# Performance work log

Measured on AMD Instinct MI355X. Metric: run time of the kernel, lower is better.

The kernel has to match this reference:

```python
import jax, jax.numpy as jnp
import numpy as np

G_RATIO = 0.5
TMAX = 0.25
TB_FACTOR = 0.001


def conv2d(x, w, b):
    # x: [B,C,H,W], w: [O,C,kh,kw]
    y = jax.lax.conv_general_dilated(x, w, (1, 1), 'SAME',
                                     dimension_numbers=('NCHW', 'OIHW', 'NCHW'))
    return y + b[None, :, None, None]


def encoder(inputs, w1, b1, w2, b2):
    # simplified cost-map encoder standing in for smp.Unet; outputs sigmoid cost map [B,1,H,W]
    h = jax.nn.relu(conv2d(inputs, w1, b1))
    return jax.nn.sigmoid(conv2d(h, w2, b2))


def get_heuristic(goal_maps, tb_factor=TB_FACTOR):
    # goal_maps: [B,H,W] one-hot
    B, H, W = goal_maps.shape
    yy, xx = jnp.meshgrid(jnp.arange(H), jnp.arange(W), indexing='ij')
    loc = jnp.stack([yy, xx], 0).astype(goal_maps.dtype)          # [2,H,W]
    goal_loc = jnp.einsum('kij,bij->bk', loc, goal_maps)           # [B,2]
    d = jnp.abs(loc[None] - goal_loc[:, :, None, None])            # [B,2,H,W]
    h = d.min(axis=1) + d.max(axis=1)                              # chebyshev-style
    euc = jnp.sqrt((d ** 2).sum(axis=1))
    return h + tb_factor * euc


def st_softmax_noexp(val):
    # straight-through hard selection of the max-probability node
    B = val.shape[0]
    v = val.reshape(B, -1)
    y = v / v.sum(-1, keepdims=True)
    ind = jnp.argmax(y, axis=-1)
    y_hard = jax.nn.one_hot(ind, y.shape[-1], dtype=y.dtype)
    return (jax.lax.stop_gradient(y_hard - y) + y).reshape(val.shape)


def backtrack(start_maps, goal_maps, parents, current_t):
    B, H, W = start_maps.shape
    par = jax.lax.stop_gradient(parents).astype(jnp.int32)         # [B,HW]
    goal_flat = goal_maps.reshape(B, -1).astype(jnp.int32)
    path = goal_flat
    loc = (par * goal_flat).sum(-1)                                # parent of goal node
    rng = jnp.arange(B)

    def body(i, carry):
        path, loc = carry
        path = path.at[rng, loc].set(1)
        loc = par[rng, loc]
        return (path, loc)

    path, _ = jax.lax.fori_loop(0, current_t, body, (path, loc))
    return path.reshape(B, H, W).astype(jnp.float32)


def differentiable_astar(cost_maps, start_maps, goal_maps, obstacles_maps):
    cost = cost_maps[:, 0]
    start = start_maps[:, 0]
    goal = goal_maps[:, 0]
    obs = obstacles_maps[:, 0]
    B, H, W = cost.shape

    # Moore (8-neighbor) expansion filter: 3x3 ones with zero center
    nf = jnp.ones((1, 1, 3, 3), cost.dtype).at[0, 0, 1, 1].set(0.0)

    def expand(x):  # x: [B,H,W]
        return jax.lax.conv_general_dilated(x[:, None], nf, (1, 1), 'SAME',
                                            dimension_numbers=('NCHW', 'OIHW', 'NCHW'))[:, 0]

    h = get_heuristic(goal) + cost
    size = W
    steps = int(TMAX * H * W)
    inv_sqrt = 1.0 / np.sqrt(size)

    goal_idx = jnp.argmax(goal.reshape(B, -1), -1).astype(cost.dtype)
    parents0 = jnp.broadcast_to(goal_idx[:, None], (B, H * W)).astype(cost.dtype)
    one = jnp.asarray(1.0, cost.dtype)

    def step(carry, _):
        g, open_m, hist, parents = carry
        f = G_RATIO * g + (1.0 - G_RATIO) * h
        f_exp = jnp.exp(-f * inv_sqrt) * open_m
        sel = st_softmax_noexp(f_exp)                              # [B,H,W]

        dist_to_goal = (sel * goal).sum((1, 2), keepdims=True)
        is_unsolved = (dist_to_goal < 1e-8).astype(cost.dtype)

        hist = jnp.clip(hist + sel, 0.0, 1.0)
        open_m = jnp.clip(open_m - is_unsolved * sel, 0.0, 1.0)

        nbr = expand(sel) * obs
        g2 = expand((g + cost) * sel)
        idx = ((one - open_m) * (one - hist) + open_m * (g > g2).astype(cost.dtype)) * nbr
        idx = jax.lax.stop_gradient(idx)
        g = g2 * idx + g * (one - idx)
        g = jax.lax.stop_gradient(g)                               # detach_g=True
        open_m = jax.lax.stop_gradient(jnp.clip(open_m + idx, 0.0, 1.0))

        idx_f = idx.reshape(B, -1)
        new_par = jnp.argmax(sel.reshape(B, -1), -1).astype(cost.dtype)[:, None]
        parents = new_par * idx_f + parents * (one - idx_f)
        return (g, open_m, hist, parents), None

    init = (jnp.zeros_like(cost), start, jnp.zeros_like(cost), parents0)
    (g, open_m, hist, parents), _ = jax.lax.scan(step, init, None, length=steps)

    paths = backtrack(start, goal, parents, steps - 1)
    return hist[:, None], paths[:, None]


def setup_inputs() -> dict:
    key = jax.random.key(0)
    k1, k2, k3, k4, k5 = jax.random.split(key, 5)
    B, H, W = 64, 32, 32
    maps = (jax.random.uniform(k1, (B, 1, H, W)) > 0.15).astype(jnp.float32)  # 1 = free
    sidx = jax.random.randint(k2, (B,), 0, H * W)
    gidx = jax.random.randint(k3, (B,), 0, H * W)
    start = jax.nn.one_hot(sidx, H * W, dtype=jnp.float32).reshape(B, 1, H, W)
    goal = jax.nn.one_hot(gidx, H * W, dtype=jnp.float32).reshape(B, 1, H, W)
    maps = jnp.clip(maps + start + goal, 0.0, 1.0)  # ensure start/goal are free
    w1 = jax.random.normal(k4, (32, 2, 3, 3), jnp.float32) * 0.1
    b1 = jnp.zeros((32,), jnp.float32)
    w2 = jax.random.normal(k5, (1, 32, 3, 3), jnp.float32) * 0.1
    b2 = jnp.zeros((1,), jnp.float32)
    return {"map_designs": maps, "start_maps": start, "goal_maps": goal,
            "w1": w1, "b1": b1, "w2": w2, "b2": b2}


def reference(map_designs, start_maps, goal_maps, w1, b1, w2, b2):
    # encoder_input='m+': concat map with start+goal
    inputs = jnp.concatenate([map_designs, start_maps + goal_maps], axis=1)
    pred_cost_maps = encoder(inputs, w1, b1, w2, b2)
    obstacles_maps = map_designs  # ignore_obstacles=True, learn_obstacles=False
    histories, paths = differentiable_astar(pred_cost_maps, start_maps, goal_maps, obstacles_maps)
    return histories, paths, pred_cost_maps
```

## Files before the change

kernel.cpp:

```cpp
#include <hip/hip_runtime.h>


#define HW 1024

#define DPPMAX32(v, ctrl) do {                                                 \
    unsigned int _s = (unsigned int)__builtin_amdgcn_update_dpp(               \
        (int)(v), (int)(v), (ctrl), 0xf, 0xf, false);                          \
    (v) = (_s > (v)) ? _s : (v);                                               \
} while (0)

#define PAIR_FIX(a_) { bool _r = vr[2*(a_)+1] > vr[2*(a_)];                    \
    pv[(a_)] = _r ? vr[2*(a_)+1] : vr[2*(a_)];                                 \
    pj[(a_)] = _r ? (unsigned)(2*(a_)+1) : (unsigned)(2*(a_)); }
#define QUAD_FIX(q_) { bool _r = pv[2*(q_)+1] > pv[2*(q_)];                    \
    qv[(q_)] = _r ? pv[2*(q_)+1] : pv[2*(q_)];                                 \
    qj[(q_)] = _r ? pj[2*(q_)+1] : pj[2*(q_)]; }
#define OCT_FIX(o_) { bool _r = qv[2*(o_)+1] > qv[2*(o_)];                     \
    ov[(o_)] = _r ? qv[2*(o_)+1] : qv[2*(o_)];                                 \
    oj[(o_)] = _r ? qj[2*(o_)+1] : qj[2*(o_)]; }
#define ROOT_FIX() { bool _r = ov[1] > ov[0];                                  \
    rv = _r ? ov[1] : ov[0]; rj = _r ? oj[1] : oj[0]; }

#define ASTAR_ARM(J) {                                                         \
    constexpr int JN = ((J) < 15) ? (J) + 1 : 15;                              \
    const float gj0 = gr[(J)], hj0v = hr[(J)], cj0 = cr[(J)];                  \
    const float gj1 = gr[JN],  hj1v = hr[JN],  cj1 = cr[JN];                   \
    float gselv = jS_is_j0 ? gj0 : gj1;                                        \
    float cselv = jS_is_j0 ? cj0 : cj1;                                        \
    float gs = __uint_as_float((unsigned int)__builtin_amdgcn_readlane(        \
        (int)__float_as_uint(gselv), owner));                                  \
    float cs = __uint_as_float((unsigned int)__builtin_amdgcn_readlane(        \
        (int)__float_as_uint(cselv), owner));                                  \
    const float gsum = gs + cs;            \
    const float gA = vjA_is_j0 ? gj0 : gj1;                                    \
    const float hA = vjA_is_j0 ? hj0v : hj1v;                                  \
    const float gB = jP_is_j0 ? gj0 : gj1;                                     \
    const float hB = jP_is_j0 ? hj0v : hj1v;                                   \
    idxA = canAn || (canAr && (gA > gsum));                                    \
    idxB = canBn || (canBr && (gB > gsum));                                    \
    float fA = 0.5f * (gsum + hA);                                             \
    unsigned int nvA = __float_as_uint(expf(__fmul_rn(-fA, C_INV)));           \
    float fB = 0.5f * (gsum + hB);                                             \
    unsigned int nvB = __float_as_uint(expf(__fmul_rn(-fB, C_INV)));           \
    const bool uA0 = idxA && vjA_is_j0, uB0 = idxB && jP_is_j0;                \
    const bool uA1 = idxA && !vjA_is_j0, uB1 = idxB && !jP_is_j0;              \
    const bool u0 = uA0 || uB0, u1 = uA1 || uB1;                               \
    if (u0) { gr[(J)] = gsum; vr[(J)] = uA0 ? nvA : nvB; }                     \
    if (u1) { gr[JN]  = gsum; vr[JN]  = uA1 ? nvA : nvB; }                     \
    if (closeU &&  jS_is_j0) vr[(J)] = 0u;                                     \
    if (closeU && !jS_is_j0) vr[JN]  = 0u;                                     \
    constexpr int pa = (J) >> 1, pb = JN >> 1;                                 \
    PAIR_FIX(pa);                                                              \
    if constexpr (pb != pa) PAIR_FIX(pb);                                      \
    constexpr int qa = pa >> 1, qb = pb >> 1;                                  \
    QUAD_FIX(qa);                                                              \
    if constexpr (qb != qa) QUAD_FIX(qb);                                      \
    constexpr int oa = qa >> 1, ob = qb >> 1;                                  \
    OCT_FIX(oa);                                                               \
    if constexpr (ob != oa) OCT_FIX(ob);                                       \
    ROOT_FIX();                                                                \
  }

__global__ __launch_bounds__(256) void fused_nastar(
    const float* __restrict__ maps, const float* __restrict__ start,
    const float* __restrict__ goal, const float* __restrict__ w1,
    const float* __restrict__ b1, const float* __restrict__ w2,
    const float* __restrict__ b2, float* __restrict__ out_hist,
    float* __restrict__ out_path, float* __restrict__ out_cost) {
  __shared__ float hid[8][HW];
  __shared__ float c_l[HW];
  __shared__ unsigned short par[HW];
  __shared__ unsigned char path_sh[HW];
  __shared__ unsigned int hist_lds[64];

  const int t = threadIdx.x;
  const int b = blockIdx.x;
  const float C_INV = 0.17677669529663687f;

  const float* m_p = maps  + b * HW;
  const float* s_p = start + b * HW;
  const float* g_p = goal  + b * HW;

  float acc2[4] = {b2[0], b2[0], b2[0], b2[0]};
  for (int grp = 0; grp < 4; ++grp) {
    #pragma unroll
    for (int p = 0; p < 4; ++p) {
      int pix = p * 256 + t;
      int y = pix >> 5, x = pix & 31;
      float win0[9], win1[9];
      #pragma unroll
      for (int ky = 0; ky < 3; ++ky) {
        #pragma unroll
        for (int kx = 0; kx < 3; ++kx) {
          int yy = y + ky - 1, xx = x + kx - 1;
          bool ok = (yy >= 0) && (yy <= 31) && (xx >= 0) && (xx <= 31);
          int q = ok ? yy * 32 + xx : 0;
          float v0 = m_p[q];
          float v1 = s_p[q] + g_p[q];
          win0[ky * 3 + kx] = ok ? v0 : 0.0f;
          win1[ky * 3 + kx] = ok ? v1 : 0.0f;
        }
      }
      #pragma unroll
      for (int ocl = 0; ocl < 8; ++ocl) {
        int oc = grp * 8 + ocl;
        const float* w = w1 + oc * 18;
        float acc = b1[oc];
        #pragma unroll
        for (int k = 0; k < 9; ++k) {
          acc += win0[k] * w[k];
          acc += win1[k] * w[9 + k];
        }
        hid[ocl][pix] = fmaxf(acc, 0.0f);
      }
    }
    __syncthreads();
    #pragma unroll
    for (int p = 0; p < 4; ++p) {
      int pix = p * 256 + t;
      int y = pix >> 5, x = pix & 31;
      float a = acc2[p];
      #pragma unroll
      for (int ocl = 0; ocl < 8; ++ocl) {
        int ic = grp * 8 + ocl;
        const float* w = w2 + ic * 9;
        #pragma unroll
        for (int ky = 0; ky < 3; ++ky) {
          #pragma unroll
          for (int kx = 0; kx < 3; ++kx) {
            int yy = y + ky - 1, xx = x + kx - 1;
            bool ok = (yy >= 0) && (yy <= 31) && (xx >= 0) && (xx <= 31);
            int q = ok ? yy * 32 + xx : 0;
            float hv = hid[ocl][q];
            a += (ok ? hv : 0.0f) * w[ky * 3 + kx];
          }
        }
      }
      acc2[p] = a;
    }
    __syncthreads();
  }
  #pragma unroll
  for (int p = 0; p < 4; ++p) {
    int pix = p * 256 + t;
    float c = 1.0f / (1.0f + expf(-acc2[p]));
    c_l[pix] = c;
    out_cost[b * HW + pix] = c;
  }
  __syncthreads();

  if (t < 64) {
    const int lane = t;
    reinterpret_cast<int4*>(path_sh)[lane] = make_int4(0, 0, 0, 0);
    int myg = -1;
    #pragma unroll
    for (int j = 0; j < 16; ++j) {
      int cell = j * 64 + lane;
      if (g_p[cell] > 0.5f) myg = cell;
    }
    unsigned long long gm = __ballot(myg >= 0);
    int src_lane = (int)__ffsll(gm) - 1;
    const int goal_idx = __shfl(myg, src_lane, 64);
    const int gy = goal_idx >> 5, gx = goal_idx & 31;

    unsigned int open_m = 0, hist_m = 0, obs_m = 0;
    float gr[16], hr[16], cr[16];
    unsigned int vr[16];
    #pragma unroll
    for (int j = 0; j < 16; ++j) {
      int cell = j * 64 + lane;
      int y = cell >> 5, x = cell & 31;
      float cst = c_l[cell];
      cr[j] = cst;
      int dy = y - gy; dy = dy < 0 ? -dy : dy;
      int dx = x - gx; dx = dx < 0 ? -dx : dx;
      float e = sqrtf((float)(dy * dy + dx * dx));
      float heur = __fadd_rn((float)(dy + dx), __fmul_rn(0.001f, e));
      float hc = __fadd_rn(heur, cst);
      hr[j] = hc;
      gr[j] = 0.0f;
      bool isobs = (m_p[cell] != 0.0f);
      bool isst  = (s_p[cell] > 0.5f);
      if (isobs) obs_m  |= 1u << j;
      if (isst)  open_m |= 1u << j;
      float f = 0.5f * (0.0f + hc);
      float ex = expf(__fmul_rn(-f, C_INV));
      vr[j] = isst ? __float_as_uint(ex) : 0u;
      par[cell] = (unsigned short)goal_idx;
    }

    unsigned int pv[8], pj[8], qv[4], qj[4], ov[2], oj[2], rv, rj;
    #pragma unroll
    for (int a = 0; a < 8; ++a) PAIR_FIX(a);
    #pragma unroll
    for (int q = 0; q < 4; ++q) QUAD_FIX(q);
    #pragma unroll
    for (int o = 0; o < 2; ++o) OCT_FIX(o);
    ROOT_FIX();

    const int x = lane & 31, half = lane >> 5;
    const unsigned int lowbase = 1023u - (unsigned)lane;

    for (int step = 0; step < 256; ++step) {
      unsigned int vmx = rv;
      DPPMAX32(vmx, 0x111);
      DPPMAX32(vmx, 0x112);
      DPPMAX32(vmx, 0x114);
      DPPMAX32(vmx, 0x118);
      DPPMAX32(vmx, 0x142);
      DPPMAX32(vmx, 0x143);
      const unsigned int svmax =
          (unsigned int)__builtin_amdgcn_readlane((int)vmx, 63);

      const unsigned long long tied = __ballot(rv == svmax);
      int sel_;
      if (__popcll(tied) == 1) {
        const int wl = (int)__ffsll(tied) - 1;
        const unsigned int rjw =
            (unsigned int)__builtin_amdgcn_readlane((int)rj, wl);
        sel_ = (int)((rjw << 6) | (unsigned)wl);
      } else {
        unsigned int lo = (rv == svmax) ? (lowbase - (rj << 6)) : 0u;
        DPPMAX32(lo, 0x111);
        DPPMAX32(lo, 0x112);
        DPPMAX32(lo, 0x114);
        DPPMAX32(lo, 0x118);
        DPPMAX32(lo, 0x142);
        DPPMAX32(lo, 0x143);
        const unsigned int klo =
            (unsigned int)__builtin_amdgcn_readlane((int)lo, 63);
        sel_ = 1023 - (int)klo;
      }
      const int sel = __builtin_amdgcn_readfirstlane(sel_);
      const int jsel = sel >> 6, owner = sel & 63;
      const int ys = sel >> 5, xs = sel & 31;
      const bool unsolved = (sel != goal_idx);

      const int j0 = (ys > 0 ? ys - 1 : 0) >> 1;
      const int jP = (ys < 31 ? ys + 1 : 31) >> 1;
      const bool jS_is_j0 = (jsel == j0);
      const bool jP_is_j0 = (jP == j0);

      int dxs = x - xs; int adx = dxs < 0 ? -dxs : dxs;
      const bool act = (adx <= 1);
      const bool samep = (((ys ^ half) & 1) == 0);
      const int yA = samep ? ys : (ys - 1);
      const bool vAv = act && (samep ? (adx >= 1) : (yA >= 0));
      const int yB = ys + 1;
      const bool vBv = act && (!samep) && (yB <= 31);
      const int cA = vAv ? (yA * 32 + x) : 0;
      const int cB = vBv ? (yB * 32 + x) : 0;
      const int vjA = samep ? jsel : j0;
      const bool vjA_is_j0 = (!samep) || jS_is_j0;

      bool obA = (obs_m  >> (vjA & 15)) & 1;
      bool opA = (open_m >> (vjA & 15)) & 1;
      bool hiA = (hist_m >> (vjA & 15)) & 1;
      bool obB = (obs_m  >> (jP & 15)) & 1;
      bool opB = (open_m >> (jP & 15)) & 1;
      bool hiB = (hist_m >> (jP & 15)) & 1;
      const bool canAn = vAv && obA && !opA && !hiA;
      const bool canAr = vAv && obA && opA;
      const bool canBn = vBv && obB && !opB && !hiB;
      const bool canBr = vBv && obB && opB;

      const bool ownerlane = (lane == owner);
      const bool closeU = unsolved && ownerlane;
      const bool histnew = ownerlane && !((hist_m >> (jsel & 15)) & 1);
      const bool opencl  = closeU && ((open_m >> (jsel & 15)) & 1);

      bool idxA = false, idxB = false;

      if (j0 < 8) {
        if (j0 < 4) {
          if (j0 < 2) { if (j0 == 0) ASTAR_ARM(0) else ASTAR_ARM(1) }
          else        { if (j0 == 2) ASTAR_ARM(2) else ASTAR_ARM(3) }
        } else {
          if (j0 < 6) { if (j0 == 4) ASTAR_ARM(4) else ASTAR_ARM(5) }
          else        { if (j0 == 6) ASTAR_ARM(6) else ASTAR_ARM(7) }
        }
      } else {
        if (j0 < 12) {
          if (j0 < 10) { if (j0 == 8)  ASTAR_ARM(8)  else ASTAR_ARM(9)  }
          else         { if (j0 == 10) ASTAR_ARM(10) else ASTAR_ARM(11) }
        } else {
          if (j0 < 14) { if (j0 == 12) ASTAR_ARM(12) else ASTAR_ARM(13) }
          else         { if (j0 == 14) ASTAR_ARM(14) else ASTAR_ARM(15) }
        }
      }

      if (idxA) par[cA] = (unsigned short)sel;
      if (idxB) par[cB] = (unsigned short)sel;

      hist_m |= ownerlane ? (1u << (jsel & 15)) : 0u;
      unsigned int clr = closeU ? (1u << (jsel & 15)) : 0u;
      unsigned int aA  = idxA ? (1u << (vjA & 15)) : 0u;
      unsigned int aB  = idxB ? (1u << (jP & 15)) : 0u;
      open_m = (open_m & ~clr) | aA | aB;

      unsigned long long anych = __ballot(idxA || idxB || histnew || opencl);
      if (anych == 0ull) break;
    }

    hist_lds[lane] = hist_m;

    if (lane == 0) {
      path_sh[goal_idx] = 1;
      int loc = par[goal_idx];
      for (int i = 0; i < 255; ++i) {
        if (path_sh[loc]) break;
        path_sh[loc] = 1;
        loc = par[loc];
      }
    }
  }
  __syncthreads();

  const int base = t * 4;
  float hv[4], pvv[4];
  #pragma unroll
  for (int p = 0; p < 4; ++p) {
    int cell = base + p;
    hv[p] = (float)((hist_lds[cell & 63] >> (cell >> 6)) & 1);
    pvv[p] = (float)path_sh[cell];
  }
  *reinterpret_cast<float4*>(out_hist + b * HW + base) =
      make_float4(hv[0], hv[1], hv[2], hv[3]);
  *reinterpret_cast<float4*>(out_path + b * HW + base) =
      make_float4(pvv[0], pvv[1], pvv[2], pvv[3]);
}

extern "C" void kernel_launch(void* const* d_in, const int* in_sizes, int n_in,
                              void* d_out, int out_size, void* d_ws, size_t ws_size,
                              hipStream_t stream) {
  (void)in_sizes; (void)n_in; (void)d_ws; (void)ws_size; (void)out_size;
  const float* maps  = (const float*)d_in[0];
  const float* start = (const float*)d_in[1];
  const float* goal  = (const float*)d_in[2];
  const float* w1    = (const float*)d_in[3];
  const float* b1    = (const float*)d_in[4];
  const float* w2    = (const float*)d_in[5];
  const float* b2    = (const float*)d_in[6];

  float* out      = (float*)d_out;
  float* out_hist = out;
  float* out_path = out + 64 * HW;
  float* out_cost = out + 128 * HW;

  fused_nastar<<<64, 256, 0, stream>>>(maps, start, goal, w1, b1, w2, b2,
                                       out_hist, out_path, out_cost);
}
```

Before: 144.2 us.

## Keep A* parent pointers in registers and backtrack via wave readlane

Parent indices move out of LDS into per-lane registers, updated inside the unrolled A* arm. This removes the per-iteration shared-memory scatter stores. Backtracking now packs the 16 parents into 10-bit fields, reads each parent with readlane, and stores path membership as bitmasks instead of a byte array. The g+c add is also fused before a single readlane rather than two. The trade is more VGPR pressure and a serial backtrack made of readlane chains.

```diff
diff --git a/kernel.cpp b/kernel.cpp
--- a/kernel.cpp
+++ b/kernel.cpp
@@ -25,13 +25,11 @@
     constexpr int JN = ((J) < 15) ? (J) + 1 : 15;                              \
     const float gj0 = gr[(J)], hj0v = hr[(J)], cj0 = cr[(J)];                  \
     const float gj1 = gr[JN],  hj1v = hr[JN],  cj1 = cr[JN];                   \
-    float gselv = jS_is_j0 ? gj0 : gj1;                                        \
-    float cselv = jS_is_j0 ? cj0 : cj1;                                        \
-    float gs = __uint_as_float((unsigned int)__builtin_amdgcn_readlane(        \
-        (int)__float_as_uint(gselv), owner));                                  \
-    float cs = __uint_as_float((unsigned int)__builtin_amdgcn_readlane(        \
-        (int)__float_as_uint(cselv), owner));                                  \
-    const float gsum = gs + cs;            \
+                 \
+    float gcs = (jS_is_j0 ? gj0 : gj1) + (jS_is_j0 ? cj0 : cj1);               \
+    const float gsum = __uint_as_float(                                        \
+        (unsigned int)__builtin_amdgcn_readlane(                               \
+            (int)__float_as_uint(gcs), owner));                                \
     const float gA = vjA_is_j0 ? gj0 : gj1;                                    \
     const float hA = vjA_is_j0 ? hj0v : hj1v;                                  \
     const float gB = jP_is_j0 ? gj0 : gj1;                                     \
@@ -45,8 +43,10 @@
     const bool uA0 = idxA && vjA_is_j0, uB0 = idxB && jP_is_j0;                \
     const bool uA1 = idxA && !vjA_is_j0, uB1 = idxB && !jP_is_j0;              \
     const bool u0 = uA0 || uB0, u1 = uA1 || uB1;                               \
-    if (u0) { gr[(J)] = gsum; vr[(J)] = uA0 ? nvA : nvB; }                     \
-    if (u1) { gr[JN]  = gsum; vr[JN]  = uA1 ? nvA : nvB; }                     \
+    if (u0) { gr[(J)] = gsum; vr[(J)] = uA0 ? nvA : nvB;                       \
+              par_r[(J)] = (unsigned)sel; }                                    \
+    if (u1) { gr[JN]  = gsum; vr[JN]  = uA1 ? nvA : nvB;                       \
+              par_r[JN] = (unsigned)sel; }                                     \
     if (closeU &&  jS_is_j0) vr[(J)] = 0u;                                     \
     if (closeU && !jS_is_j0) vr[JN]  = 0u;                                     \
     constexpr int pa = (J) >> 1, pb = JN >> 1;                                 \
@@ -69,9 +69,8 @@
     float* __restrict__ out_path, float* __restrict__ out_cost) {
   __shared__ float hid[8][HW];
   __shared__ float c_l[HW];
-  __shared__ unsigned short par[HW];
-  __shared__ unsigned char path_sh[HW];
   __shared__ unsigned int hist_lds[64];
+  __shared__ unsigned int path_lds[64];
 
   const int t = threadIdx.x;
   const int b = blockIdx.x;
@@ -151,7 +150,6 @@
 
   if (t < 64) {
     const int lane = t;
-    reinterpret_cast<int4*>(path_sh)[lane] = make_int4(0, 0, 0, 0);
     int myg = -1;
     #pragma unroll
     for (int j = 0; j < 16; ++j) {
@@ -166,6 +164,7 @@
     unsigned int open_m = 0, hist_m = 0, obs_m = 0;
     float gr[16], hr[16], cr[16];
     unsigned int vr[16];
+    unsigned int par_r[16];
     #pragma unroll
     for (int j = 0; j < 16; ++j) {
       int cell = j * 64 + lane;
@@ -186,7 +185,7 @@
       float f = 0.5f * (0.0f + hc);
       float ex = expf(__fmul_rn(-f, C_INV));
       vr[j] = isst ? __float_as_uint(ex) : 0u;
-      par[cell] = (unsigned short)goal_idx;
+      par_r[j] = (unsigned)goal_idx;
     }
 
     unsigned int pv[8], pj[8], qv[4], qj[4], ov[2], oj[2], rv, rj;
@@ -248,8 +247,6 @@
       const bool vAv = act && (samep ? (adx >= 1) : (yA >= 0));
       const int yB = ys + 1;
       const bool vBv = act && (!samep) && (yB <= 31);
-      const int cA = vAv ? (yA * 32 + x) : 0;
-      const int cB = vBv ? (yB * 32 + x) : 0;
       const int vjA = samep ? jsel : j0;
       const bool vjA_is_j0 = (!samep) || jS_is_j0;
 
@@ -289,9 +286,6 @@
         }
       }
 
-      if (idxA) par[cA] = (unsigned short)sel;
-      if (idxB) par[cB] = (unsigned short)sel;
-
       hist_m |= ownerlane ? (1u << (jsel & 15)) : 0u;
       unsigned int clr = closeU ? (1u << (jsel & 15)) : 0u;
       unsigned int aA  = idxA ? (1u << (vjA & 15)) : 0u;
@@ -304,15 +298,40 @@
 
     hist_lds[lane] = hist_m;
 
-    if (lane == 0) {
-      path_sh[goal_idx] = 1;
-      int loc = par[goal_idx];
-      for (int i = 0; i < 255; ++i) {
-        if (path_sh[loc]) break;
-        path_sh[loc] = 1;
-        loc = par[loc];
-      }
-    }
+    unsigned int pp[6] = {0u, 0u, 0u, 0u, 0u, 0u};
+    #pragma unroll
+    for (int j = 0; j < 16; ++j) {
+      const unsigned bp = (unsigned)j * 10u;
+      const unsigned w = bp >> 5, s = bp & 31u;
+      pp[w] |= par_r[j] << s;
+      if (s > 22u) pp[w + 1] |= par_r[j] >> (32u - s);
+    }
+
+    auto extract_par = [&](int c) -> int {
+      const int jq = c >> 6, ownq = c & 63;
+      const unsigned bp = (unsigned)jq * 10u;
+      const unsigned w = bp >> 5, s = bp & 31u;
+      unsigned lo = (w == 0u) ? pp[0] : (w == 1u) ? pp[1]
+                  : (w == 2u) ? pp[2] : (w == 3u) ? pp[3] : pp[4];
+      unsigned hi = (w == 0u) ? pp[1] : (w == 1u) ? pp[2]
+                  : (w == 2u) ? pp[3] : (w == 3u) ? pp[4] : pp[5];
+      unsigned long long both = ((unsigned long long)hi << 32) | lo;
+      unsigned ext = (unsigned)(both >> s) & 1023u;
+      return (int)__builtin_amdgcn_readlane((int)ext, ownq);
+    };
+
+    unsigned int path_m = 0u;
+    if (lane == (goal_idx & 63)) path_m |= 1u << (goal_idx >> 6);
+    int loc = extract_par(goal_idx);
+    for (int i = 0; i < 255; ++i) {
+      const int jc = loc >> 6, ow = loc & 63;
+      const unsigned pm =
+          (unsigned)__builtin_amdgcn_readlane((int)path_m, ow);
+      if ((pm >> jc) & 1u) break;
+      if (lane == ow) path_m |= 1u << jc;
+      loc = extract_par(loc);
+    }
+    path_lds[lane] = path_m;
   }
   __syncthreads();
 
@@ -321,8 +340,8 @@
   #pragma unroll
   for (int p = 0; p < 4; ++p) {
     int cell = base + p;
-    hv[p] = (float)((hist_lds[cell & 63] >> (cell >> 6)) & 1);
-    pvv[p] = (float)path_sh[cell];
+    hv[p]  = (float)((hist_lds[cell & 63] >> (cell >> 6)) & 1);
+    pvv[p] = (float)((path_lds[cell & 63] >> (cell >> 6)) & 1);
   }
   *reinterpret_cast<float4*>(out_hist + b * HW + base) =
       make_float4(hv[0], hv[1], hv[2], hv[3]);
```

After: 152.6 us. 1.06x slower.
